# Performance work log

Measured on AMD Instinct MI355X. Metric: run time of the kernel, lower is better.

The kernel has to match this reference:

```python
import jax, jax.numpy as jnp
import numpy as np

B, N_CLASS, N_CENTER, HIDDEN = 1024, 50, 8, 512
INIT_MU, BETA, EPS = 0.1, 0.5, 1e-8


def setup_inputs() -> dict:
    key = jax.random.key(0)
    k1, k2, k3, k4 = jax.random.split(key, 4)
    x = jax.random.normal(k1, (B, HIDDEN), dtype=jnp.float32)
    # class_mu ~ U(-init_mu, init_mu), matching torch.rand(...) * 2*init_mu - init_mu
    class_mu = jax.random.uniform(k2, (N_CLASS, N_CENTER, HIDDEN),
                                  minval=-INIT_MU, maxval=INIT_MU, dtype=jnp.float32)
    # binary dropout-style mask: (rand > beta).float()
    mask = (jax.random.uniform(k3, (N_CENTER, HIDDEN)) > BETA).astype(jnp.float32)
    # fixed random projection W ~ 0.1 * N(0,1)
    W = jax.random.normal(k4, (HIDDEN, HIDDEN), dtype=jnp.float32) * 0.1
    return {"x": x, "class_mu": class_mu, "mask": mask, "W": W}


def reference(x, class_mu, mask, W):
    # [B, n_center, hidden]: per-center masked copy of x, then shared projection W
    masked = x[:, None, :] * mask[None, :, :]
    mul = jnp.einsum('bch,hd->bcd', masked, W)
    # broadcast squared-distance against cluster centers: [B, n_class, n_center]
    diff = mul[:, None, :, :] - class_mu[None, :, :, :]  # [B, K, C, H]
    score = 1.0 / (1.0 + jnp.sum(diff * diff, axis=-1))  # Student-t style kernel
    # normalize over n_center (dim 2)
    distances = score / (jnp.sum(score, axis=2, keepdims=True) + EPS)
    # k_assign: second normalization over last dim (n_center)
    k_assign = distances / jnp.sum(distances, axis=-1, keepdims=True)
    return (mul, k_assign, distances)
```

## Files before the change

kernel.cpp:

```cpp
#include <hip/hip_runtime.h>

typedef short s16x8 __attribute__((ext_vector_type(8)));
typedef float f32x4 __attribute__((ext_vector_type(4)));
typedef unsigned int u32x4 __attribute__((ext_vector_type(4)));

#define NB      1024
#define NCLASS  50
#define NCENTER 8
#define HID     512
#define KPAD    64

#define OFF_XBF    0u
#define OFF_MASK16 1048576u
#define OFF_WT     1056768u
#define OFF_MUBF   1581056u
#define OFF_MUNT   2105344u
#define OFF_MULBF  2107392u
#define OFF_RNORM  10496000u

#define OUT_KA 4194304
#define OUT_D  4603904

__device__ __forceinline__ short f2bf(float f) {
    unsigned int u = __float_as_uint(f);
    unsigned int r = (u + 0x7FFFu + ((u >> 16) & 1u)) >> 16;
    return (short)(unsigned short)r;
}

__global__ __launch_bounds__(256) void prep_kernel(
    const float* __restrict__ x, const float* __restrict__ class_mu,
    const float* __restrict__ mask, const float* __restrict__ W,
    short* __restrict__ xbf, short* __restrict__ mask16, short* __restrict__ WT,
    short* __restrict__ Mubf, float* __restrict__ MunormT,
    float* __restrict__ rowNorm)
{
    __shared__ float lds[64][65];
    const int blk = blockIdx.x, tid = threadIdx.x;

    if (blk < 32) {
        #pragma unroll
        for (int i = 0; i < 8; ++i) {
            int g = (blk * 256 + tid) + i * 8192;
            int e = g * 8;
            const float4* xp = (const float4*)(x + e);
            float4 a = xp[0], b = xp[1];
            s16x8 o;
            o[0] = f2bf(a.x); o[1] = f2bf(a.y); o[2] = f2bf(a.z); o[3] = f2bf(a.w);
            o[4] = f2bf(b.x); o[5] = f2bf(b.y); o[6] = f2bf(b.z); o[7] = f2bf(b.w);
            *(s16x8*)(xbf + e) = o;
        }
    } else if (blk == 32) {
        int e = tid * 16;
        const float4* mp = (const float4*)(mask + e);
        float4 m0 = mp[0], m1 = mp[1], m2 = mp[2], m3 = mp[3];
        s16x8 o0, o1;
        o0[0] = (m0.x != 0.f) ? (short)0xFFFF : 0; o0[1] = (m0.y != 0.f) ? (short)0xFFFF : 0;
        o0[2] = (m0.z != 0.f) ? (short)0xFFFF : 0; o0[3] = (m0.w != 0.f) ? (short)0xFFFF : 0;
        o0[4] = (m1.x != 0.f) ? (short)0xFFFF : 0; o0[5] = (m1.y != 0.f) ? (short)0xFFFF : 0;
        o0[6] = (m1.z != 0.f) ? (short)0xFFFF : 0; o0[7] = (m1.w != 0.f) ? (short)0xFFFF : 0;
        o1[0] = (m2.x != 0.f) ? (short)0xFFFF : 0; o1[1] = (m2.y != 0.f) ? (short)0xFFFF : 0;
        o1[2] = (m2.z != 0.f) ? (short)0xFFFF : 0; o1[3] = (m2.w != 0.f) ? (short)0xFFFF : 0;
        o1[4] = (m3.x != 0.f) ? (short)0xFFFF : 0; o1[5] = (m3.y != 0.f) ? (short)0xFFFF : 0;
        o1[6] = (m3.z != 0.f) ? (short)0xFFFF : 0; o1[7] = (m3.w != 0.f) ? (short)0xFFFF : 0;
        *(s16x8*)(mask16 + e) = o0;
        *(s16x8*)(mask16 + e + 8) = o1;
        float4 z = {0.f, 0.f, 0.f, 0.f};
        #pragma unroll
        for (int j = 0; j < 8; ++j)
            *(float4*)(rowNorm + (j * 256 + tid) * 4) = z;
    } else if (blk < 97) {
        int t = blk - 33;
        int th = t & 7, td = t >> 3;
        int col = tid & 63, rb = tid >> 6;
        #pragma unroll
        for (int it = 0; it < 16; ++it) {
            int row = it * 4 + rb;
            lds[row][col] = W[(th * 64 + row) * HID + td * 64 + col];
        }
        __syncthreads();
        #pragma unroll
        for (int it = 0; it < 16; ++it) {
            int row = it * 4 + rb;
            WT[(td * 64 + row) * HID + th * 64 + col] = f2bf(lds[col][row]);
        }
    } else {
        int w = (blk - 97) * 4 + (tid >> 6);
        int lane = tid & 63;
        int c = w >> 6, kk = w & 63;
        int h = lane * 8;
        float v[8];
        if (kk < NCLASS) {
            const float4* p = (const float4*)(class_mu + (kk * NCENTER + c) * HID + h);
            float4 a = p[0], bq = p[1];
            v[0] = a.x;  v[1] = a.y;  v[2] = a.z;  v[3] = a.w;
            v[4] = bq.x; v[5] = bq.y; v[6] = bq.z; v[7] = bq.w;
        } else {
            #pragma unroll
            for (int j = 0; j < 8; ++j) v[j] = 0.f;
        }
        s16x8 o; float sq = 0.f;
        #pragma unroll
        for (int j = 0; j < 8; ++j) { o[j] = f2bf(v[j]); sq += v[j] * v[j]; }
        *(s16x8*)(Mubf + (c * KPAD + kk) * HID + h) = o;
        sq += __shfl_xor(sq, 1);  sq += __shfl_xor(sq, 2);  sq += __shfl_xor(sq, 4);
        sq += __shfl_xor(sq, 8);  sq += __shfl_xor(sq, 16); sq += __shfl_xor(sq, 32);
        if (lane == 0) MunormT[kk * 8 + c] = sq;
    }
}

__global__ __launch_bounds__(256) void gemm_mul(
    const short* __restrict__ xbf, const short* __restrict__ mask16,
    const short* __restrict__ WT,
    float* __restrict__ mul_out, short* __restrict__ mulbf,
    float* __restrict__ rowNorm)
{
    __shared__ short As[128 * 32];
    __shared__ short Bs[128 * 32];
    const int tid = threadIdx.x;
    const int bm = blockIdx.x * 128;
    const int bn = blockIdx.y * 128;
    const int wave = tid >> 6, lane = tid & 63;
    const int wm = (wave & 1) * 64, wn = (wave >> 1) * 64;
    const int q = lane >> 4, l16 = lane & 15;

    f32x4 acc[4][4] = {};

    const int r0 = tid >> 2, c0 = (tid & 3) * 8;
    const int bA0 = (bm >> 3) + (r0 >> 3);
    const int bA1 = (bm >> 3) + ((r0 + 64) >> 3);
    const int cA  = r0 & 7;

    for (int it = 0; it < 16; ++it) {
        const int k0 = it * 32;
        u32x4 ma = *(const u32x4*)(mask16 + cA * HID + k0 + c0);
        u32x4 x0 = *(const u32x4*)(xbf + bA0 * HID + k0 + c0);
        u32x4 x1 = *(const u32x4*)(xbf + bA1 * HID + k0 + c0);
        *(u32x4*)(As + r0 * 32 + c0)        = x0 & ma;
        *(u32x4*)(As + (r0 + 64) * 32 + c0) = x1 & ma;
        *(s16x8*)(Bs + r0 * 32 + c0)        = *(const s16x8*)(WT + (bn + r0) * HID + k0 + c0);
        *(s16x8*)(Bs + (r0 + 64) * 32 + c0) = *(const s16x8*)(WT + (bn + r0 + 64) * HID + k0 + c0);
        __syncthreads();

        s16x8 af[4], bfr[4];
        #pragma unroll
        for (int mt = 0; mt < 4; ++mt)
            af[mt] = *(const s16x8*)(As + (wm + mt * 16 + l16) * 32 + q * 8);
        #pragma unroll
        for (int nt = 0; nt < 4; ++nt)
            bfr[nt] = *(const s16x8*)(Bs + (wn + nt * 16 + l16) * 32 + q * 8);
        #pragma unroll
        for (int mt = 0; mt < 4; ++mt)
            #pragma unroll
            for (int nt = 0; nt < 4; ++nt)
                acc[mt][nt] = __builtin_amdgcn_mfma_f32_16x16x32_bf16(af[mt], bfr[nt], acc[mt][nt], 0, 0, 0);
        __syncthreads();
    }

    #pragma unroll
    for (int mt = 0; mt < 4; ++mt) {
        #pragma unroll
        for (int nt = 0; nt < 4; ++nt) {
            #pragma unroll
            for (int reg = 0; reg < 4; ++reg) {
                int gr = bm + wm + mt * 16 + q * 4 + reg;
                int gc = bn + wn + nt * 16 + l16;
                float v = acc[mt][nt][reg];
                mul_out[gr * HID + gc] = v;
                mulbf[gr * HID + gc] = f2bf(v);
            }
        }
    }
    #pragma unroll
    for (int mt = 0; mt < 4; ++mt) {
        #pragma unroll
        for (int reg = 0; reg < 4; ++reg) {
            float s = acc[mt][0][reg] * acc[mt][0][reg];
            s += acc[mt][1][reg] * acc[mt][1][reg];
            s += acc[mt][2][reg] * acc[mt][2][reg];
            s += acc[mt][3][reg] * acc[mt][3][reg];
            s += __shfl_xor(s, 1); s += __shfl_xor(s, 2);
            s += __shfl_xor(s, 4); s += __shfl_xor(s, 8);
            if (l16 == 0)
                atomicAdd(&rowNorm[bm + wm + mt * 16 + q * 4 + reg], s);
        }
    }
}

__global__ __launch_bounds__(64) void scorenorm_kernel(
    const short* __restrict__ mulbf, const short* __restrict__ Mubf,
    const float* __restrict__ MunormT, const float* __restrict__ rowNorm,
    float* __restrict__ out)
{
    const int bt = blockIdx.x & 63, cg = blockIdx.x >> 6;
    const int lane = threadIdx.x & 63;
    const int q = lane >> 4, l16 = lane & 15;
    const int b0 = bt * 16, cls0 = cg * 16;

    f32x4 acc[8] = {};
    const short* arow = mulbf + (b0 + l16) * NCENTER * HID + q * 8;
    const short* brow = Mubf + (cls0 + l16) * HID + q * 8;

    for (int it = 0; it < 16; ++it) {
        const int k0 = it * 32;
        s16x8 av[8], bv[8];
        #pragma unroll
        for (int c = 0; c < 8; ++c) av[c] = *(const s16x8*)(arow + c * HID + k0);
        #pragma unroll
        for (int c = 0; c < 8; ++c) bv[c] = *(const s16x8*)(brow + c * KPAD * HID + k0);
        #pragma unroll
        for (int c = 0; c < 8; ++c)
            acc[c] = __builtin_amdgcn_mfma_f32_16x16x32_bf16(av[c], bv[c], acc[c], 0, 0, 0);
    }

    const int cls = cls0 + l16;
    float4 mn0 = *(const float4*)(MunormT + cls * 8);
    float4 mn1 = *(const float4*)(MunormT + cls * 8 + 4);
    const float mn[8] = {mn0.x, mn0.y, mn0.z, mn0.w, mn1.x, mn1.y, mn1.z, mn1.w};

    #pragma unroll
    for (int reg = 0; reg < 4; ++reg) {
        const int b = b0 + q * 4 + reg;
        float4 rn0 = *(const float4*)(rowNorm + b * 8);
        float4 rn1 = *(const float4*)(rowNorm + b * 8 + 4);
        const float rn[8] = {rn0.x, rn0.y, rn0.z, rn0.w, rn1.x, rn1.y, rn1.z, rn1.w};
        float sc[8], S = 0.f;
        #pragma unroll
        for (int c = 0; c < 8; ++c) {
            float sq = rn[c] + mn[c] - 2.f * acc[c][reg];
            sc[c] = 1.f / (1.f + sq);
            S += sc[c];
        }
        float invk = 1.f / S;
        float invd = 1.f / (S + 1e-8f);
        if (cls < NCLASS) {
            float* kap = out + OUT_KA + (b * NCLASS + cls) * NCENTER;
            float* dp  = out + OUT_D  + (b * NCLASS + cls) * NCENTER;
            float4 o;
            o.x = sc[0] * invk; o.y = sc[1] * invk; o.z = sc[2] * invk; o.w = sc[3] * invk;
            ((float4*)kap)[0] = o;
            o.x = sc[4] * invk; o.y = sc[5] * invk; o.z = sc[6] * invk; o.w = sc[7] * invk;
            ((float4*)kap)[1] = o;
            o.x = sc[0] * invd; o.y = sc[1] * invd; o.z = sc[2] * invd; o.w = sc[3] * invd;
            ((float4*)dp)[0] = o;
            o.x = sc[4] * invd; o.y = sc[5] * invd; o.z = sc[6] * invd; o.w = sc[7] * invd;
            ((float4*)dp)[1] = o;
        }
    }
}

extern "C" void kernel_launch(void* const* d_in, const int* in_sizes, int n_in,
                              void* d_out, int out_size, void* d_ws, size_t ws_size,
                              hipStream_t stream) {
    const float* x        = (const float*)d_in[0];
    const float* class_mu = (const float*)d_in[1];
    const float* mask     = (const float*)d_in[2];
    const float* W        = (const float*)d_in[3];
    float* out = (float*)d_out;
    char* ws = (char*)d_ws;

    short* xbf     = (short*)(ws + OFF_XBF);
    short* mask16  = (short*)(ws + OFF_MASK16);
    short* WT      = (short*)(ws + OFF_WT);
    short* Mubf    = (short*)(ws + OFF_MUBF);
    float* MunormT = (float*)(ws + OFF_MUNT);
    short* mulbf   = (short*)(ws + OFF_MULBF);
    float* rowNorm = (float*)(ws + OFF_RNORM);

    prep_kernel<<<225, 256, 0, stream>>>(x, class_mu, mask, W,
                                         xbf, mask16, WT, Mubf, MunormT, rowNorm);
    gemm_mul<<<dim3(64, 4), 256, 0, stream>>>(xbf, mask16, WT, out, mulbf, rowNorm);
    scorenorm_kernel<<<256, 64, 0, stream>>>(mulbf, Mubf, MunormT, rowNorm, out);
}
```

Before: 101.6 us.

## Drop LDS staging in mul GEMM and use single-wave 64x64 tiles

The projection GEMM now runs one wave per 64x64 output tile. Each wave loads its bf16 x (masked in registers) and W fragments straight from global memory into MFMA operands, with no shared-memory staging and no barriers. The grid grows from 256 to 1024 blocks to spread work across more CUs, and the squared-norm reduction is folded into the store loop. In exchange there is no cross-wave reuse through LDS, so global and L2 traffic for W and x goes up.

```diff
diff --git a/kernel.cpp b/kernel.cpp
--- a/kernel.cpp
+++ b/kernel.cpp
@@ -108,80 +108,61 @@
     }
 }
 
-__global__ __launch_bounds__(256) void gemm_mul(
+__global__ __launch_bounds__(64) void gemm_mul(
     const short* __restrict__ xbf, const short* __restrict__ mask16,
     const short* __restrict__ WT,
     float* __restrict__ mul_out, short* __restrict__ mulbf,
     float* __restrict__ rowNorm)
 {
-    __shared__ short As[128 * 32];
-    __shared__ short Bs[128 * 32];
-    const int tid = threadIdx.x;
-    const int bm = blockIdx.x * 128;
-    const int bn = blockIdx.y * 128;
-    const int wave = tid >> 6, lane = tid & 63;
-    const int wm = (wave & 1) * 64, wn = (wave >> 1) * 64;
+    const int lane = threadIdx.x;
     const int q = lane >> 4, l16 = lane & 15;
+    const int bm = blockIdx.x * 64, bn = blockIdx.y * 64;
+    const int c = l16 & 7;
+    const int bglob = (bm >> 3) + (l16 >> 3);
 
     f32x4 acc[4][4] = {};
 
-    const int r0 = tid >> 2, c0 = (tid & 3) * 8;
-    const int bA0 = (bm >> 3) + (r0 >> 3);
-    const int bA1 = (bm >> 3) + ((r0 + 64) >> 3);
-    const int cA  = r0 & 7;
+    const short* xp = xbf + bglob * HID + q * 8;
+    const short* mp = mask16 + c * HID + q * 8;
+    const short* wp = WT + (bn + l16) * HID + q * 8;
 
     for (int it = 0; it < 16; ++it) {
         const int k0 = it * 32;
-        u32x4 ma = *(const u32x4*)(mask16 + cA * HID + k0 + c0);
-        u32x4 x0 = *(const u32x4*)(xbf + bA0 * HID + k0 + c0);
-        u32x4 x1 = *(const u32x4*)(xbf + bA1 * HID + k0 + c0);
-        *(u32x4*)(As + r0 * 32 + c0)        = x0 & ma;
-        *(u32x4*)(As + (r0 + 64) * 32 + c0) = x1 & ma;
-        *(s16x8*)(Bs + r0 * 32 + c0)        = *(const s16x8*)(WT + (bn + r0) * HID + k0 + c0);
-        *(s16x8*)(Bs + (r0 + 64) * 32 + c0) = *(const s16x8*)(WT + (bn + r0 + 64) * HID + k0 + c0);
-        __syncthreads();
-
-        s16x8 af[4], bfr[4];
-        #pragma unroll
-        for (int mt = 0; mt < 4; ++mt)
-            af[mt] = *(const s16x8*)(As + (wm + mt * 16 + l16) * 32 + q * 8);
+        u32x4 mf = *(const u32x4*)(mp + k0);
+        s16x8 af[4], bf[4];
+        #pragma unroll
+        for (int mt = 0; mt < 4; ++mt) {
+            u32x4 xv = *(const u32x4*)(xp + 2 * mt * HID + k0);
+            u32x4 av = xv & mf;
+            af[mt] = *(s16x8*)&av;
+        }
         #pragma unroll
         for (int nt = 0; nt < 4; ++nt)
-            bfr[nt] = *(const s16x8*)(Bs + (wn + nt * 16 + l16) * 32 + q * 8);
+            bf[nt] = *(const s16x8*)(wp + nt * 16 * HID + k0);
         #pragma unroll
         for (int mt = 0; mt < 4; ++mt)
             #pragma unroll
             for (int nt = 0; nt < 4; ++nt)
-                acc[mt][nt] = __builtin_amdgcn_mfma_f32_16x16x32_bf16(af[mt], bfr[nt], acc[mt][nt], 0, 0, 0);
-        __syncthreads();
+                acc[mt][nt] = __builtin_amdgcn_mfma_f32_16x16x32_bf16(af[mt], bf[nt], acc[mt][nt], 0, 0, 0);
     }
 
     #pragma unroll
     for (int mt = 0; mt < 4; ++mt) {
         #pragma unroll
-        for (int nt = 0; nt < 4; ++nt) {
+        for (int reg = 0; reg < 4; ++reg) {
+            const int gr = bm + mt * 16 + q * 4 + reg;
+            float s = 0.f;
             #pragma unroll
-            for (int reg = 0; reg < 4; ++reg) {
-                int gr = bm + wm + mt * 16 + q * 4 + reg;
-                int gc = bn + wn + nt * 16 + l16;
+            for (int nt = 0; nt < 4; ++nt) {
                 float v = acc[mt][nt][reg];
+                int gc = bn + nt * 16 + l16;
                 mul_out[gr * HID + gc] = v;
                 mulbf[gr * HID + gc] = f2bf(v);
+                s += v * v;
             }
-        }
-    }
-    #pragma unroll
-    for (int mt = 0; mt < 4; ++mt) {
-        #pragma unroll
-        for (int reg = 0; reg < 4; ++reg) {
-            float s = acc[mt][0][reg] * acc[mt][0][reg];
-            s += acc[mt][1][reg] * acc[mt][1][reg];
-            s += acc[mt][2][reg] * acc[mt][2][reg];
-            s += acc[mt][3][reg] * acc[mt][3][reg];
             s += __shfl_xor(s, 1); s += __shfl_xor(s, 2);
             s += __shfl_xor(s, 4); s += __shfl_xor(s, 8);
-            if (l16 == 0)
-                atomicAdd(&rowNorm[bm + wm + mt * 16 + q * 4 + reg], s);
+            if (l16 == 0) atomicAdd(&rowNorm[gr], s);
         }
     }
 }
@@ -268,6 +249,6 @@
 
     prep_kernel<<<225, 256, 0, stream>>>(x, class_mu, mask, W,
                                          xbf, mask16, WT, Mubf, MunormT, rowNorm);
-    gemm_mul<<<dim3(64, 4), 256, 0, stream>>>(xbf, mask16, WT, out, mulbf, rowNorm);
+    gemm_mul<<<dim3(128, 8), 64, 0, stream>>>(xbf, mask16, WT, out, mulbf, rowNorm);
     scorenorm_kernel<<<256, 64, 0, stream>>>(mulbf, Mubf, MunormT, rowNorm, out);
 }
```

After: 103.4 us. Within noise of the previous version (+1.7%).
